# Performance work log

Hardware: AMD Instinct MI355X
Metric: run time of the kernel (lower is better)

Reference implementation:

```python
import jax, jax.numpy as jnp
import numpy as np

SNR_LIN = 10.0          # 10**(snrdb/10), snrdb=10
NUM_TX_STREAMS = 1
A_INFO, B_INFO = 0.83, 0.73
ER, MOD = 0.25, 4
SUBCARRIERS_PER_RB = 12


def make_codebook():
    # 3GPP TS 38.214 Type-I rank-1 codebook for N_t=4 (N_1=2, N_2=1, O_1=4, O_2=1)
    N1, O1 = 2, 4
    l = np.arange(N1 * O1)          # 8 beams
    k = np.arange(N1)
    n = np.arange(4)                # QPSK cophasing
    v = np.exp(2j * np.pi * np.outer(l, k) / (O1 * N1))          # (8, 2)
    phi = np.exp(1j * np.pi * n / 2)                              # (4,)
    W = np.concatenate([np.broadcast_to(v[:, None, :], (8, 4, 2)),
                        phi[None, :, None] * v[:, None, :]], axis=-1)  # (8,4,4)
    W = W / np.sqrt(4.0)            # 1/sqrt(P_CSI_RS)
    return jnp.asarray(W.reshape(32, 4, 1), dtype=jnp.complex64)  # (C, N_t, N_s)


def setup_inputs() -> dict:
    key = jax.random.key(0)
    k1, k2 = jax.random.split(key)
    shape = (32, 1, 2, 1, 4, 14, 3072)  # [B, n_rx, N_r, n_tx, N_t, S, F]
    return {
        "h_est_real": jax.random.normal(k1, shape, dtype=jnp.float32),
        "h_est_imag": jax.random.normal(k2, shape, dtype=jnp.float32),
    }


def _per_rb_rate(h_real, h_imag, cb):
    beta = 4.4492 * ER ** 2 + 4.5655 * ER + 1.2982  # EESM beta for mod=4
    h = (h_real + 1j * h_imag).astype(jnp.complex64)
    # rb_mapper: average groups of 12 subcarriers into RBs along last axis
    nrb = h.shape[-1] // SUBCARRIERS_PER_RB
    h = h[..., : nrb * SUBCARRIERS_PER_RB]
    h = h.reshape(h.shape[:-1] + (nrb, SUBCARRIERS_PER_RB)).mean(-1)
    # (B, n_rx, n_tx, S, RB, N_r, N_t)
    ht = jnp.transpose(h, (0, 1, 3, 5, 6, 2, 4))
    # effective channel for ALL 32 candidates at once: (C, B, n_rx, n_tx, S, RB, N_r, N_s)
    heff = jnp.einsum('...rt,cts->c...rs', ht, cb)
    hhh = jnp.einsum('c...rs,c...qs->c...rq', heff, jnp.conj(heff))  # H H^H
    tr = jnp.trace(hhh, axis1=-2, axis2=-1)
    sig_pow = jnp.abs(tr.reshape(tr.shape[0], -1).mean(-1))          # (C,)
    n_var = sig_pow / SNR_LIN                                        # (C,)
    nvM = n_var.astype(jnp.complex64).reshape((-1,) + (1,) * (hhh.ndim - 1))
    M = hhh / NUM_TX_STREAMS + nvM   # scalar added to every entry (as in source)
    # Q_ij = h_i^H M h_j
    Q = jnp.einsum('c...ri,c...rq,c...qj->c...ij', jnp.conj(heff), M, heff)
    diagQ = jnp.diagonal(Q, axis1=-2, axis2=-1)                      # (..., N_s)
    numerator = jnp.abs(diagQ) ** 2
    MMH = jnp.einsum('c...rp,c...qp->c...rq', M, jnp.conj(M))        # M M^H
    real_part = jnp.real(jnp.einsum('c...ri,c...rq,c...qi->c...i',
                                    jnp.conj(heff), MMH, heff))
    interference = jnp.sum(jnp.abs(Q) ** 2, axis=-1) - jnp.abs(diagQ) ** 2
    nvs = n_var.reshape((-1,) + (1,) * (numerator.ndim - 1))
    sinr = numerator / (nvs * real_part + interference)  # (C,B,n_rx,n_tx,S,RB,N_s)
    # EESM average over batch/rx/tx/symbol axes -> (C, RB, N_s)
    Nn = sinr.shape[1] * sinr.shape[2] * sinr.shape[3] * sinr.shape[4]
    exp_sum = jnp.exp(-sinr / beta).sum(axis=(1, 2, 3, 4)) / Nn
    avg_sinr = -beta * jnp.log(exp_sum)
    rate = (A_INFO * jnp.log2(1.0 + B_INFO * avg_sinr)).sum(-1)      # (C, RB)
    return rate.T                                                    # (RB, C)


def reference(h_est_real, h_est_imag):
    cb = make_codebook()
    per_precoder_rate = _per_rb_rate(h_est_real, h_est_imag, cb)     # (RB, C)
    PMI = jnp.argmax(per_precoder_rate, axis=1)                      # (RB,)
    rate_for_selected = jnp.max(per_precoder_rate, axis=1)           # (RB,)
    precoding_matrices = cb[PMI][None]                               # (1, RB, N_t, N_s)
    return PMI, rate_for_selected, precoding_matrices
```

## Files before the change

### kernel.cpp

```cpp
#include <hip/hip_runtime.h>
#include <math.h>

#define NU 32
#define NSYM 14
#define NSC 3072
#define NRB 256
#define NUS 448
#define NPOINT 114688
#define PLANE 114688
#define NC 32

#define BETA 2.71765f
#define INV_BETA (1.0f/2.71765f)


__global__ __launch_bounds__(256) void k1_rbavg(const float* __restrict__ hre,
                                                const float* __restrict__ him,
                                                float2* __restrict__ hrb,
                                                float* __restrict__ G) {
    __shared__ float2 tile[14][65];

    const int b = blockIdx.x;
    const int chunk = b & 3;
    const int uk = b >> 2;
    const int k = uk & 7;
    const int u = uk >> 3;
    const int rb0 = chunk * 64;
    const int tid = threadIdx.x;

    if (b == 0 && tid < 16) G[tid] = 0.0f;

    const int rb = tid & 63;
    const int s0 = tid >> 6;
    const size_t base_uk = (size_t)uk * (size_t)(NSYM * NSC);

    for (int sym = s0; sym < NSYM; sym += 4) {
        size_t base = base_uk + (size_t)sym * NSC + (size_t)(rb0 + rb) * 12;
        const float4* pr = (const float4*)(hre + base);
        const float4* pi = (const float4*)(him + base);
        float4 r0 = pr[0], r1 = pr[1], r2 = pr[2];
        float4 i0 = pi[0], i1 = pi[1], i2 = pi[2];
        float sre = ((r0.x + r0.y) + (r0.z + r0.w) + (r1.x + r1.y) +
                     (r1.z + r1.w) + (r2.x + r2.y) + (r2.z + r2.w)) * (1.0f / 12.0f);
        float sim = ((i0.x + i0.y) + (i0.z + i0.w) + (i1.x + i1.y) +
                     (i1.z + i1.w) + (i2.x + i2.y) + (i2.z + i2.w)) * (1.0f / 12.0f);
        tile[sym][rb] = make_float2(sre, sim);
    }
    __syncthreads();

    for (int w = tid; w < 64 * NSYM; w += 256) {
        int rbw = w / NSYM;
        int sym = w - rbw * NSYM;
        int idx2 = k * PLANE + (rb0 + rbw) * NUS + u * NSYM + sym;
        hrb[idx2] = tile[sym][rbw];
    }
}

__global__ __launch_bounds__(256) void k2_gram(const float2* __restrict__ hrb,
                                               float* __restrict__ G) {
    const int p = blockIdx.x * 256 + threadIdx.x;
    float2 x[8];
#pragma unroll
    for (int k = 0; k < 8; k++) x[k] = hrb[k * PLANE + p];

    float acc[16];
#pragma unroll
    for (int t = 0; t < 4; t++) {
        acc[t] = x[t].x * x[t].x + x[t].y * x[t].y +
                 x[4 + t].x * x[4 + t].x + x[4 + t].y * x[4 + t].y;
    }
    const int pa[6] = {0, 0, 0, 1, 1, 2};
    const int pb[6] = {1, 2, 3, 2, 3, 3};
#pragma unroll
    for (int q = 0; q < 6; q++) {
        int a = pa[q], bb = pb[q];
        float re = x[a].x * x[bb].x + x[a].y * x[bb].y +
                   x[4 + a].x * x[4 + bb].x + x[4 + a].y * x[4 + bb].y;
        float im = x[a].y * x[bb].x - x[a].x * x[bb].y +
                   x[4 + a].y * x[4 + bb].x - x[4 + a].x * x[4 + bb].y;
        acc[4 + 2 * q] = re;
        acc[5 + 2 * q] = im;
    }

#pragma unroll
    for (int m = 1; m < 64; m <<= 1) {
#pragma unroll
        for (int i = 0; i < 16; i++) acc[i] += __shfl_xor(acc[i], m);
    }

    __shared__ float red[4][16];
    const int lane = threadIdx.x & 63;
    const int wv = threadIdx.x >> 6;
    if (lane == 0) {
#pragma unroll
        for (int i = 0; i < 16; i++) red[wv][i] = acc[i];
    }
    __syncthreads();
    if (threadIdx.x < 16) {
        float v = red[0][threadIdx.x] + red[1][threadIdx.x] +
                  red[2][threadIdx.x] + red[3][threadIdx.x];
        atomicAdd(&G[threadIdx.x], v);
    }
}

__global__ __launch_bounds__(512) void k3_rate(const float2* __restrict__ hrb,
                                               const float* __restrict__ G,
                                               float* __restrict__ out,
                                               int out_size) {
    __shared__ float2 tile[NUS * 9];
    __shared__ float nv_s[NC];
    __shared__ float cbr_s[NC][4], cbi_s[NC][4];
    __shared__ float rate_s[NC];

    const int rb = blockIdx.x;
    const int tid = threadIdx.x;

    if (tid < NC) {
        const int l = tid >> 2, n = tid & 3;
        float wr, wi;
        const float SQ = 0.70710678118654752f;
        switch (l) {
            case 0: wr = 1.f;  wi = 0.f;  break;
            case 1: wr = SQ;   wi = SQ;   break;
            case 2: wr = 0.f;  wi = 1.f;  break;
            case 3: wr = -SQ;  wi = SQ;   break;
            case 4: wr = -1.f; wi = 0.f;  break;
            case 5: wr = -SQ;  wi = -SQ;  break;
            case 6: wr = 0.f;  wi = -1.f; break;
            default: wr = SQ;  wi = -SQ;  break;
        }
        float phr = (n == 0) ? 1.f : (n == 2) ? -1.f : 0.f;
        float phi = (n == 1) ? 1.f : (n == 3) ? -1.f : 0.f;
        cbr_s[tid][0] = 1.f;  cbi_s[tid][0] = 0.f;
        cbr_s[tid][1] = wr;   cbi_s[tid][1] = wi;
        cbr_s[tid][2] = phr;  cbi_s[tid][2] = phi;
        cbr_s[tid][3] = phr * wr - phi * wi;
        cbi_s[tid][3] = phr * wi + phi * wr;

        float s = G[0] + G[1] + G[2] + G[3];
        const int pa[6] = {0, 0, 0, 1, 1, 2};
        const int pb[6] = {1, 2, 3, 2, 3, 3};
#pragma unroll
        for (int q = 0; q < 6; q++) {
            float gre = G[4 + 2 * q], gim = G[5 + 2 * q];
            float car = cbr_s[tid][pa[q]], cai = cbi_s[tid][pa[q]];
            float cbrx = cbr_s[tid][pb[q]], cbix = cbi_s[tid][pb[q]];
            float zr = car * cbrx + cai * cbix;
            float zi = cai * cbrx - car * cbix;
            s += 2.0f * (zr * gre - zi * gim);
        }
        nv_s[tid] = s * (1.0f / (114688.0f * 10.0f));
    }

    for (int idx = tid; idx < NUS * 8; idx += 512) {
        int k = idx / NUS;
        int us = idx - k * NUS;
        tile[us * 9 + k] = hrb[k * PLANE + rb * NUS + us];
    }
    __syncthreads();

    const int c = tid >> 4;
    const int j = tid & 15;
    float cr[4], ci[4];
#pragma unroll
    for (int t = 0; t < 4; t++) { cr[t] = cbr_s[c][t]; ci[t] = cbi_s[c][t]; }
    const float nv = nv_s[c];

    float sum = 0.0f;
    for (int us = j; us < NUS; us += 16) {
        const float2* pt = &tile[us * 9];
        float h0r = 0.f, h0i = 0.f, h1r = 0.f, h1i = 0.f;
#pragma unroll
        for (int t = 0; t < 4; t++) {
            float2 a0 = pt[t], a1 = pt[4 + t];
            h0r += cr[t] * a0.x - ci[t] * a0.y;
            h0i += cr[t] * a0.y + ci[t] * a0.x;
            h1r += cr[t] * a1.x - ci[t] * a1.y;
            h1i += cr[t] * a1.y + ci[t] * a1.x;
        }
        float a = h0r * h0r + h0i * h0i + h1r * h1r + h1i * h1i;
        float Sr = h0r + h1r, Si = h0i + h1i;
        float p = Sr * Sr + Si * Si;
        float Q = a * a + nv * p;
        float den = nv * (a * a * a + 2.0f * a * nv * p + 2.0f * nv * nv * p);
        float sinr = (Q * Q) / den;
        sum += expf(-sinr * INV_BETA);
    }
#pragma unroll
    for (int m = 8; m >= 1; m >>= 1) sum += __shfl_xor(sum, m, 16);

    if (j == 0) {
        float es = sum * (1.0f / 448.0f);
        float avg = -BETA * logf(es);
        rate_s[c] = 0.83f * log2f(1.0f + 0.73f * avg);
    }
    __syncthreads();

    if (tid == 0) {
        float best = rate_s[0];
        int bc = 0;
        for (int cc = 1; cc < NC; cc++) {
            if (rate_s[cc] > best) { best = rate_s[cc]; bc = cc; }
        }
        if (rb < out_size) out[rb] = (float)bc;
        if (NRB + rb < out_size) out[NRB + rb] = best;

        if (out_size >= 2 * NRB + 8 * NRB) {
#pragma unroll
            for (int t = 0; t < 4; t++) {
                int o = 2 * NRB + (rb * 4 + t) * 2;
                out[o] = 0.5f * cbr_s[bc][t];
                out[o + 1] = 0.5f * cbi_s[bc][t];
            }
        } else {
#pragma unroll
            for (int t = 0; t < 4; t++) {
                int o = 2 * NRB + rb * 4 + t;
                if (o < out_size) out[o] = 0.5f * cbr_s[bc][t];
            }
        }
    }
}

extern "C" void kernel_launch(void* const* d_in, const int* in_sizes, int n_in,
                              void* d_out, int out_size, void* d_ws, size_t ws_size,
                              hipStream_t stream) {
    const float* hre = (const float*)d_in[0];
    const float* him = (const float*)d_in[1];
    float* out = (float*)d_out;

    float* ws = (float*)d_ws;
    float* G = ws;
    float2* hrb = (float2*)(ws + 64);

    k1_rbavg<<<1024, 256, 0, stream>>>(hre, him, hrb, G);
    k2_gram<<<448, 256, 0, stream>>>(hrb, G);
    k3_rate<<<256, 512, 0, stream>>>(hrb, G, out, out_size);
}
```

Measured before the change: 128.4 us.

## Fuse RB averaging with Gram accumulation and replace atomics with per-block partials

Merges the RB-averaging and Gram-reduction kernels, so each block computes the Gram contributions straight from its shared-memory tile instead of rereading the averaged channel from global memory in a separate launch. The block layout changes so that each block holds all 8 antenna planes for 16 RBs and one user. Each block writes its 16 partial sums to a buffer rather than using atomics, and every rate block re-reduces all 512 partials. This removes one launch and one pass over the intermediate, at the cost of redundant partial reduction in each of the 256 rate blocks and fewer, heavier k1 blocks.

```diff
diff --git a/kernel.cpp b/kernel.cpp
--- a/kernel.cpp
+++ b/kernel.cpp
@@ -6,35 +6,35 @@
 #define NSC 3072
 #define NRB 256
 #define NUS 448
-#define NPOINT 114688
 #define PLANE 114688
 #define NC 32
 
 #define BETA 2.71765f
 #define INV_BETA (1.0f/2.71765f)
 
-
-__global__ __launch_bounds__(256) void k1_rbavg(const float* __restrict__ hre,
+#define CRB 16
+#define TP 17
+#define TR (NSYM*TP)
+
+
+__global__ __launch_bounds__(256) void k1_fused(const float* __restrict__ hre,
                                                 const float* __restrict__ him,
                                                 float2* __restrict__ hrb,
-                                                float* __restrict__ G) {
-    __shared__ float2 tile[14][65];
-
-    const int b = blockIdx.x;
-    const int chunk = b & 3;
-    const int uk = b >> 2;
-    const int k = uk & 7;
-    const int u = uk >> 3;
-    const int rb0 = chunk * 64;
+                                                float* __restrict__ partials) {
+    __shared__ float2 tile[8 * TR];
+    __shared__ float red[4][16];
+
     const int tid = threadIdx.x;
-
-    if (b == 0 && tid < 16) G[tid] = 0.0f;
-
-    const int rb = tid & 63;
-    const int s0 = tid >> 6;
-    const size_t base_uk = (size_t)uk * (size_t)(NSYM * NSC);
-
-    for (int sym = s0; sym < NSYM; sym += 4) {
+    const int u = blockIdx.x >> 4;
+    const int rb0 = (blockIdx.x & 15) * CRB;
+
+    const int rb = tid & 15;
+    const int k = (tid >> 4) & 7;
+    const int half = tid >> 7;
+    const size_t base_uk = (size_t)(u * 8 + k) * (size_t)(NSYM * NSC);
+
+    for (int m = 0; m < 7; m++) {
+        const int sym = half * 7 + m;
         size_t base = base_uk + (size_t)sym * NSC + (size_t)(rb0 + rb) * 12;
         const float4* pr = (const float4*)(hre + base);
         const float4* pi = (const float4*)(him + base);
@@ -44,42 +44,45 @@
                      (r1.z + r1.w) + (r2.x + r2.y) + (r2.z + r2.w)) * (1.0f / 12.0f);
         float sim = ((i0.x + i0.y) + (i0.z + i0.w) + (i1.x + i1.y) +
                      (i1.z + i1.w) + (i2.x + i2.y) + (i2.z + i2.w)) * (1.0f / 12.0f);
-        tile[sym][rb] = make_float2(sre, sim);
-    }
-    __syncthreads();
-
-    for (int w = tid; w < 64 * NSYM; w += 256) {
-        int rbw = w / NSYM;
-        int sym = w - rbw * NSYM;
-        int idx2 = k * PLANE + (rb0 + rbw) * NUS + u * NSYM + sym;
-        hrb[idx2] = tile[sym][rbw];
-    }
-}
-
-__global__ __launch_bounds__(256) void k2_gram(const float2* __restrict__ hrb,
-                                               float* __restrict__ G) {
-    const int p = blockIdx.x * 256 + threadIdx.x;
-    float2 x[8];
-#pragma unroll
-    for (int k = 0; k < 8; k++) x[k] = hrb[k * PLANE + p];
-
-    float acc[16];
-#pragma unroll
-    for (int t = 0; t < 4; t++) {
-        acc[t] = x[t].x * x[t].x + x[t].y * x[t].y +
-                 x[4 + t].x * x[4 + t].x + x[4 + t].y * x[4 + t].y;
-    }
+        tile[k * TR + sym * TP + rb] = make_float2(sre, sim);
+    }
+    __syncthreads();
+
+    for (int idx = tid; idx < 8 * CRB * NSYM; idx += 256) {
+        int kk = idx / (CRB * NSYM);
+        int rem = idx - kk * (CRB * NSYM);
+        int rbw = rem / NSYM;
+        int sym = rem - rbw * NSYM;
+        hrb[kk * PLANE + (rb0 + rbw) * NUS + u * NSYM + sym] =
+            tile[kk * TR + sym * TP + rbw];
+    }
+
     const int pa[6] = {0, 0, 0, 1, 1, 2};
     const int pb[6] = {1, 2, 3, 2, 3, 3};
-#pragma unroll
-    for (int q = 0; q < 6; q++) {
-        int a = pa[q], bb = pb[q];
-        float re = x[a].x * x[bb].x + x[a].y * x[bb].y +
-                   x[4 + a].x * x[4 + bb].x + x[4 + a].y * x[4 + bb].y;
-        float im = x[a].y * x[bb].x - x[a].x * x[bb].y +
-                   x[4 + a].y * x[4 + bb].x - x[4 + a].x * x[4 + bb].y;
-        acc[4 + 2 * q] = re;
-        acc[5 + 2 * q] = im;
+    float acc[16];
+#pragma unroll
+    for (int i = 0; i < 16; i++) acc[i] = 0.0f;
+
+    if (tid < CRB * NSYM) {
+        const int sym = tid >> 4;
+        const int prb = tid & 15;
+        float2 x[8];
+#pragma unroll
+        for (int kk = 0; kk < 8; kk++) x[kk] = tile[kk * TR + sym * TP + prb];
+
+#pragma unroll
+        for (int t = 0; t < 4; t++) {
+            acc[t] = x[t].x * x[t].x + x[t].y * x[t].y +
+                     x[4 + t].x * x[4 + t].x + x[4 + t].y * x[4 + t].y;
+        }
+#pragma unroll
+        for (int q = 0; q < 6; q++) {
+            int a = pa[q], bb = pb[q];
+            acc[4 + 2 * q] = x[a].x * x[bb].x + x[a].y * x[bb].y +
+                             x[4 + a].x * x[4 + bb].x + x[4 + a].y * x[4 + bb].y;
+            acc[5 + 2 * q] = x[a].y * x[bb].x - x[a].x * x[bb].y +
+                             x[4 + a].y * x[4 + bb].x - x[4 + a].x * x[4 + bb].y;
+        }
     }
 
 #pragma unroll
@@ -87,33 +90,38 @@
 #pragma unroll
         for (int i = 0; i < 16; i++) acc[i] += __shfl_xor(acc[i], m);
     }
-
-    __shared__ float red[4][16];
-    const int lane = threadIdx.x & 63;
-    const int wv = threadIdx.x >> 6;
+    const int lane = tid & 63;
+    const int wv = tid >> 6;
     if (lane == 0) {
 #pragma unroll
         for (int i = 0; i < 16; i++) red[wv][i] = acc[i];
     }
     __syncthreads();
-    if (threadIdx.x < 16) {
-        float v = red[0][threadIdx.x] + red[1][threadIdx.x] +
-                  red[2][threadIdx.x] + red[3][threadIdx.x];
-        atomicAdd(&G[threadIdx.x], v);
+    if (tid < 16) {
+        partials[blockIdx.x * 16 + tid] =
+            red[0][tid] + red[1][tid] + red[2][tid] + red[3][tid];
     }
 }
 
 __global__ __launch_bounds__(512) void k3_rate(const float2* __restrict__ hrb,
-                                               const float* __restrict__ G,
+                                               const float* __restrict__ partials,
                                                float* __restrict__ out,
                                                int out_size) {
     __shared__ float2 tile[NUS * 9];
+    __shared__ float Gs[16];
+    __shared__ float redg[16][17];
     __shared__ float nv_s[NC];
     __shared__ float cbr_s[NC][4], cbi_s[NC][4];
     __shared__ float rate_s[NC];
 
     const int rb = blockIdx.x;
     const int tid = threadIdx.x;
+
+    for (int idx = tid; idx < NUS * 8; idx += 512) {
+        int k = idx / NUS;
+        int us = idx - k * NUS;
+        tile[us * 9 + k] = hrb[k * PLANE + rb * NUS + us];
+    }
 
     if (tid < NC) {
         const int l = tid >> 2, n = tid & 3;
@@ -136,13 +144,32 @@
         cbr_s[tid][2] = phr;  cbi_s[tid][2] = phi;
         cbr_s[tid][3] = phr * wr - phi * wi;
         cbi_s[tid][3] = phr * wi + phi * wr;
-
-        float s = G[0] + G[1] + G[2] + G[3];
+    }
+
+    if (tid < 256) {
+        const int col = tid & 15;
+        const int grp = tid >> 4;
+        float s = 0.0f;
+#pragma unroll
+        for (int m = 0; m < 32; m++) s += partials[(grp * 32 + m) * 16 + col];
+        redg[grp][col] = s;
+    }
+    __syncthreads();
+    if (tid < 16) {
+        float v = 0.0f;
+#pragma unroll
+        for (int g = 0; g < 16; g++) v += redg[g][tid];
+        Gs[tid] = v;
+    }
+    __syncthreads();
+
+    if (tid < NC) {
+        float s = Gs[0] + Gs[1] + Gs[2] + Gs[3];
         const int pa[6] = {0, 0, 0, 1, 1, 2};
         const int pb[6] = {1, 2, 3, 2, 3, 3};
 #pragma unroll
         for (int q = 0; q < 6; q++) {
-            float gre = G[4 + 2 * q], gim = G[5 + 2 * q];
+            float gre = Gs[4 + 2 * q], gim = Gs[5 + 2 * q];
             float car = cbr_s[tid][pa[q]], cai = cbi_s[tid][pa[q]];
             float cbrx = cbr_s[tid][pb[q]], cbix = cbi_s[tid][pb[q]];
             float zr = car * cbrx + cai * cbix;
@@ -150,12 +177,6 @@
             s += 2.0f * (zr * gre - zi * gim);
         }
         nv_s[tid] = s * (1.0f / (114688.0f * 10.0f));
-    }
-
-    for (int idx = tid; idx < NUS * 8; idx += 512) {
-        int k = idx / NUS;
-        int us = idx - k * NUS;
-        tile[us * 9 + k] = hrb[k * PLANE + rb * NUS + us];
     }
     __syncthreads();
 
@@ -230,10 +251,9 @@
     float* out = (float*)d_out;
 
     float* ws = (float*)d_ws;
-    float* G = ws;
-    float2* hrb = (float2*)(ws + 64);
-
-    k1_rbavg<<<1024, 256, 0, stream>>>(hre, him, hrb, G);
-    k2_gram<<<448, 256, 0, stream>>>(hrb, G);
-    k3_rate<<<256, 512, 0, stream>>>(hrb, G, out, out_size);
+    float* partials = ws;
+    float2* hrb = (float2*)(ws + 8192);
+
+    k1_fused<<<512, 256, 0, stream>>>(hre, him, hrb, partials);
+    k3_rate<<<256, 512, 0, stream>>>(hrb, partials, out, out_size);
 }
```

Result: faster. 120.6 us (-6.0%).
